# Performance work log

Measured on AMD Instinct MI355X. Metric: run time of the kernel, lower is better.

Reference implementation:

```python
import jax, jax.numpy as jnp
import numpy as np
import math

B, N, F = 4, 4096, 64
NEG_SLOPE = 0.01


def _leaky_relu(x):
    return jnp.where(x >= 0, x, NEG_SLOPE * x)


def setup_inputs() -> dict:
    key = jax.random.key(0)
    k1, k2, k3, k4, k5 = jax.random.split(key, 5)
    Q = jax.random.normal(k1, (B, N, F, 2), dtype=jnp.float32)
    K = jax.random.normal(k2, (B, N, F, 2), dtype=jnp.float32)
    V = jax.random.normal(k3, (B, N, F, 2), dtype=jnp.float32)
    W_att = jax.random.normal(k4, (F, F), dtype=jnp.float32) / math.sqrt(F)
    b_att = jax.random.normal(k5, (F,), dtype=jnp.float32) * 0.01
    return {"Q": Q, "K": K, "V": V, "W_att": W_att, "b_att": b_att}


def reference(Q, K, V, W_att, b_att):
    # Split complex components: last axis is (real, imag)
    Qr, Qi = Q[..., 0], Q[..., 1]
    Kr, Ki = K[..., 0], K[..., 1]
    Vr, Vi = V[..., 0], V[..., 1]

    n = Q.shape[1]
    scale = 1.0 / math.sqrt(n)  # num_nodes == N

    # Complex scores = Q @ K^T (no conjugation, as in torch einsum on complex)
    sr = (jnp.einsum('bik,bjk->bij', Qr, Kr) - jnp.einsum('bik,bjk->bij', Qi, Ki)) * scale
    si = (jnp.einsum('bik,bjk->bij', Qr, Ki) + jnp.einsum('bik,bjk->bij', Qi, Kr)) * scale

    # Causal mask: positions j > i are masked out (contribute zero weight)
    causal = jnp.tril(jnp.ones((n, n), dtype=bool))  # [N, N], True = keep
    wr = jnp.where(causal, _leaky_relu(sr), 0.0)
    wi = jnp.where(causal, _leaky_relu(si), 0.0)

    # Attention-weighted values (real weights with real V, imag with imag V)
    out_r = jnp.einsum('bij,bjf->bif', wr, Vr)
    out_i = jnp.einsum('bij,bjf->bif', wi, Vi)

    # att_map: shared linear layer
    out_r = out_r @ W_att.T + b_att
    out_i = out_i @ W_att.T + b_att

    return jnp.stack([out_r, out_i], axis=-1)  # [B, N, F, 2]
```

## Files before the change

### kernel.cpp

```cpp
#include <hip/hip_runtime.h>

#define NB 4
#define NN 4096
#define NF 64
#define TSTEP 8
#define BLKS_PER_B 260

typedef __attribute__((ext_vector_type(8))) short bf16x8;
typedef __attribute__((ext_vector_type(4))) float f32x4;

union S8 { unsigned short u[8]; bf16x8 v; };

__device__ __forceinline__ unsigned short f2bf(float x) {
    unsigned int uu = __builtin_bit_cast(unsigned int, x);
    uu += 0x7fffu + ((uu >> 16) & 1u);
    return (unsigned short)(uu >> 16);
}

__global__ __launch_bounds__(256)
void prep_all(const float* __restrict__ Q, const float* __restrict__ K,
              const float* __restrict__ V, const float* __restrict__ W,
              short* __restrict__ QF, short* __restrict__ KF,
              short* __restrict__ VF, short* __restrict__ WF,
              float* __restrict__ out) {
    int tid = blockIdx.x * 256 + threadIdx.x;

    if (tid < 262144) {
        int sel = tid >> 17;
        int r   = tid & 0x1FFFF;
        int l  = r & 63;
        int c  = (r >> 6) & 1;
        int rg = (r >> 7) & 255;
        int b  = r >> 15;
        const float* src = sel ? K : Q;
        short*       dst = sel ? KF : QF;

        int row = rg * 16 + (l & 15);
        int k0  = c * 32 + (l >> 4) * 8;
        const float4* s4 = (const float4*)src;
        int base4 = (b * NN + row) * 32 + (k0 >> 1);

        S8 ar, ai;
        #pragma unroll
        for (int m = 0; m < 4; ++m) {
            float4 f = s4[base4 + m];
            ar.u[2 * m]     = f2bf(f.x);
            ar.u[2 * m + 1] = f2bf(f.z);
            ai.u[2 * m]     = f2bf(f.y);
            ai.u[2 * m + 1] = f2bf(f.w);
        }
        int cid0 = ((b * 256 + rg) * 2 + c) * 2;
        *(bf16x8*)(dst + (cid0 + 0) * 512 + l * 8) = ar.v;
        *(bf16x8*)(dst + (cid0 + 1) * 512 + l * 8) = ai.v;
    } else if (tid < 393216) {
        int r = tid - 262144;
        int l  = r & 63;
        int c  = (r >> 6) & 1;
        int ft = (r >> 7) & 3;
        int jt = (r >> 9) & 63;
        int b  = (r >> 15) & 3;

        int f  = ft * 16 + (l & 15);
        int j0 = jt * 64 + c * 32 + (l >> 4) * 8;
        const float2* s2 = (const float2*)V;

        S8 ar, ai;
        #pragma unroll
        for (int e = 0; e < 8; ++e) {
            float2 g = s2[(b * NN + j0 + e) * 64 + f];
            ar.u[e] = f2bf(g.x);
            ai.u[e] = f2bf(g.y);
        }
        int cid0 = (((b * 64 + jt) * 4 + ft) * 2 + c) * 2;
        *(bf16x8*)(VF + (cid0 + 0) * 512 + l * 8) = ar.v;
        *(bf16x8*)(VF + (cid0 + 1) * 512 + l * 8) = ai.v;
    } else if (tid < 393728) {
        int r = tid - 393216;
        int l  = r & 63;
        int c  = (r >> 6) & 1;
        int ft = r >> 7;
        int row = ft * 16 + (l & 15);
        int k0  = c * 32 + (l >> 4) * 8;
        const float* sp = W + row * 64 + k0;
        S8 a;
        #pragma unroll
        for (int e = 0; e < 8; ++e) a.u[e] = f2bf(sp[e]);
        *(bf16x8*)(WF + ((ft * 2 + c) * 64 + l) * 8) = a.v;
    } else {
        int r = tid - 393728;
        float4 zz = {0.f, 0.f, 0.f, 0.f};
        ((float4*)out)[r] = zz;
    }
}

__device__ __forceinline__ int tri_inv(int g) {
    int it = (int)((__builtin_sqrtf(8.0f * (float)g + 1.0f) - 1.0f) * 0.5f);
    while ((it + 1) * (it + 2) / 2 <= g) ++it;
    while (it * (it + 1) / 2 > g) --it;
    return it;
}

__global__ __launch_bounds__(256, 4)
void attn_main(const short* __restrict__ QF, const short* __restrict__ KF,
               const short* __restrict__ VF, const short* __restrict__ WF,
               const float* __restrict__ batt, float* __restrict__ out) {
    __shared__ __align__(16) unsigned short wbuf[4][2048];

    int bid = blockIdx.x;
    int b   = bid / BLKS_PER_B;
    int g   = (bid % BLKS_PER_B) * TSTEP;
    int gend = g + TSTEP;

    int w   = threadIdx.x >> 6;
    int l   = threadIdx.x & 63;
    int r16 = l & 15;
    int lb  = l >> 4;

    const f32x4 z = {0.f, 0.f, 0.f, 0.f};
    const float SCALE = 1.0f / 64.0f;
    unsigned short* wb = wbuf[w];

    while (g < gend) {
        int it   = tri_inv(g);
        int base = it * (it + 1) / 2;
        int jt0  = g - base;
        int cnt  = min(gend - g, it + 1 - jt0);
        int jt1  = jt0 + cnt;

        bf16x8 qf[2][2];
        {
            int rg = it * 4 + w;
            #pragma unroll
            for (int c = 0; c < 2; ++c)
                #pragma unroll
                for (int ch = 0; ch < 2; ++ch)
                    qf[c][ch] = *(const bf16x8*)(QF + (((b * 256 + rg) * 2 + c) * 2 + ch) * 512 + l * 8);
        }

        f32x4 o[4][2];
        #pragma unroll
        for (int ft = 0; ft < 4; ++ft) { o[ft][0] = z; o[ft][1] = z; }

        for (int jt = jt0; jt < jt1; ++jt) {
            bool diag = (jt == it);
            #pragma unroll
            for (int ct = 0; ct < 4; ++ct) {
                bf16x8 kf[2][2];
                int rg = jt * 4 + ct;
                #pragma unroll
                for (int c = 0; c < 2; ++c)
                    #pragma unroll
                    for (int ch = 0; ch < 2; ++ch)
                        kf[c][ch] = *(const bf16x8*)(KF + (((b * 256 + rg) * 2 + c) * 2 + ch) * 512 + l * 8);

                f32x4 t1 = __builtin_amdgcn_mfma_f32_16x16x32_bf16(qf[0][0], kf[0][0], z, 0, 0, 0);
                t1 = __builtin_amdgcn_mfma_f32_16x16x32_bf16(qf[1][0], kf[1][0], t1, 0, 0, 0);
                f32x4 t2 = __builtin_amdgcn_mfma_f32_16x16x32_bf16(qf[0][1], kf[0][1], z, 0, 0, 0);
                t2 = __builtin_amdgcn_mfma_f32_16x16x32_bf16(qf[1][1], kf[1][1], t2, 0, 0, 0);
                f32x4 si = __builtin_amdgcn_mfma_f32_16x16x32_bf16(qf[0][0], kf[0][1], z, 0, 0, 0);
                si = __builtin_amdgcn_mfma_f32_16x16x32_bf16(qf[1][0], kf[1][1], si, 0, 0, 0);
                si = __builtin_amdgcn_mfma_f32_16x16x32_bf16(qf[0][1], kf[0][0], si, 0, 0, 0);
                si = __builtin_amdgcn_mfma_f32_16x16x32_bf16(qf[1][1], kf[1][0], si, 0, 0, 0);

                int cH  = ct >> 1;
                int lb2 = ((ct & 1) << 1) | (r16 >> 3);
                int e   = r16 & 7;
                int base_r = (cH * 2 + 0) * 512 + lb2 * 128 + lb * 32 + e;
                int base_i = (cH * 2 + 1) * 512 + lb2 * 128 + lb * 32 + e;
                #pragma unroll
                for (int reg = 0; reg < 4; ++reg) {
                    float sr = (t1[reg] - t2[reg]) * SCALE;
                    float sv = si[reg] * SCALE;
                    float wr = sr >= 0.f ? sr : 0.01f * sr;
                    float wi = sv >= 0.f ? sv : 0.01f * sv;
                    if (diag) {
                        int ig = w * 16 + lb * 4 + reg;
                        int jg = ct * 16 + r16;
                        if (jg > ig) { wr = 0.f; wi = 0.f; }
                    }
                    wb[base_r + reg * 8] = f2bf(wr);
                    wb[base_i + reg * 8] = f2bf(wi);
                }
            }

            bf16x8 wfr[2][2];
            #pragma unroll
            for (int c = 0; c < 2; ++c)
                #pragma unroll
                for (int ch = 0; ch < 2; ++ch)
                    wfr[c][ch] = *(const bf16x8*)(wb + (c * 2 + ch) * 512 + l * 8);

            #pragma unroll
            for (int ft = 0; ft < 4; ++ft) {
                #pragma unroll
                for (int ch = 0; ch < 2; ++ch) {
                    int cid0 = (((b * 64 + jt) * 4 + ft) * 2) * 2 + ch;
                    bf16x8 v0 = *(const bf16x8*)(VF + cid0 * 512 + l * 8);
                    bf16x8 v1 = *(const bf16x8*)(VF + (cid0 + 2) * 512 + l * 8);
                    o[ft][ch] = __builtin_amdgcn_mfma_f32_16x16x32_bf16(wfr[0][ch], v0, o[ft][ch], 0, 0, 0);
                    o[ft][ch] = __builtin_amdgcn_mfma_f32_16x16x32_bf16(wfr[1][ch], v1, o[ft][ch], 0, 0, 0);
                }
            }
        }

        #pragma unroll
        for (int ft = 0; ft < 4; ++ft) {
            int cH  = ft >> 1;
            int lb2 = ((ft & 1) << 1) | (r16 >> 3);
            int e   = r16 & 7;
            #pragma unroll
            for (int ch = 0; ch < 2; ++ch) {
                int bofs = (cH * 2 + ch) * 512 + lb2 * 128 + lb * 32 + e;
                #pragma unroll
                for (int reg = 0; reg < 4; ++reg)
                    wb[bofs + reg * 8] = f2bf(o[ft][ch][reg]);
            }
        }

        bf16x8 of[2][2];
        #pragma unroll
        for (int c = 0; c < 2; ++c)
            #pragma unroll
            for (int ch = 0; ch < 2; ++ch)
                of[c][ch] = *(const bf16x8*)(wb + (c * 2 + ch) * 512 + l * 8);

        bool whole = (jt0 == 0) && (jt1 == it + 1);
        bool addb  = (jt0 == 0);
        int ibase = b * NN + it * 64 + w * 16 + lb * 4;
        #pragma unroll
        for (int ft2 = 0; ft2 < 4; ++ft2) {
            bf16x8 wa0 = *(const bf16x8*)(WF + ((ft2 * 2 + 0) * 64 + l) * 8);
            bf16x8 wa1 = *(const bf16x8*)(WF + ((ft2 * 2 + 1) * 64 + l) * 8);
            float bb = addb ? batt[ft2 * 16 + r16] : 0.f;
            #pragma unroll
            for (int ch = 0; ch < 2; ++ch) {
                f32x4 acc = __builtin_amdgcn_mfma_f32_16x16x32_bf16(of[0][ch], wa0, z, 0, 0, 0);
                acc = __builtin_amdgcn_mfma_f32_16x16x32_bf16(of[1][ch], wa1, acc, 0, 0, 0);
                #pragma unroll
                for (int reg = 0; reg < 4; ++reg) {
                    int idx = ((ibase + reg) * 64 + ft2 * 16 + r16) * 2 + ch;
                    if (whole) out[idx] = acc[reg] + bb;
                    else       atomicAdd(out + idx, acc[reg] + bb);
                }
            }
        }

        g += cnt;
    }
}

extern "C" void kernel_launch(void* const* d_in, const int* in_sizes, int n_in,
                              void* d_out, int out_size, void* d_ws, size_t ws_size,
                              hipStream_t stream) {
    const float* Q  = (const float*)d_in[0];
    const float* K  = (const float*)d_in[1];
    const float* V  = (const float*)d_in[2];
    const float* W  = (const float*)d_in[3];
    const float* bA = (const float*)d_in[4];
    float* out = (float*)d_out;

    short* QF = (short*)d_ws;
    short* KF = QF + 2097152;
    short* VF = KF + 2097152;
    short* WF = VF + 2097152;

    prep_all<<<3586, 256, 0, stream>>>(Q, K, V, W, QF, KF, VF, WF, out);
    attn_main<<<NB * BLKS_PER_B, 256, 0, stream>>>(QF, KF, VF, WF, bA, out);
}
```

Baseline: 198.3 us.

## Keep attention weights in registers via transposed MFMA operands, drop LDS staging

Swaps the MFMA operand order so the score tile comes out transposed. The leaky-relu weights and the PV output can then be packed straight into bf16 B-operand registers, with no LDS round trip, and the V and W prep layouts are permuted to match. It folds the 1/64 scale into Q during prep, uses a branch-free leaky relu, and writes output with vectorised float4 stores. It also halves the per-block tile step, doubling the block count. The aim is to remove LDS writes and reads and improve store coalescing, at the cost of more atomics from the finer split.

```diff
diff --git a/kernel.cpp b/kernel.cpp
--- a/kernel.cpp
+++ b/kernel.cpp
@@ -3,8 +3,8 @@
 #define NB 4
 #define NN 4096
 #define NF 64
-#define TSTEP 8
-#define BLKS_PER_B 260
+#define TSTEP 4
+#define BLKS_PER_B 520
 
 typedef __attribute__((ext_vector_type(8))) short bf16x8;
 typedef __attribute__((ext_vector_type(4))) float f32x4;
@@ -34,6 +34,7 @@
         int b  = r >> 15;
         const float* src = sel ? K : Q;
         short*       dst = sel ? KF : QF;
+        float sc = sel ? 1.0f : 0.015625f;
 
         int row = rg * 16 + (l & 15);
         int k0  = c * 32 + (l >> 4) * 8;
@@ -44,10 +45,10 @@
         #pragma unroll
         for (int m = 0; m < 4; ++m) {
             float4 f = s4[base4 + m];
-            ar.u[2 * m]     = f2bf(f.x);
-            ar.u[2 * m + 1] = f2bf(f.z);
-            ai.u[2 * m]     = f2bf(f.y);
-            ai.u[2 * m + 1] = f2bf(f.w);
+            ar.u[2 * m]     = f2bf(f.x * sc);
+            ar.u[2 * m + 1] = f2bf(f.z * sc);
+            ai.u[2 * m]     = f2bf(f.y * sc);
+            ai.u[2 * m + 1] = f2bf(f.w * sc);
         }
         int cid0 = ((b * 256 + rg) * 2 + c) * 2;
         *(bf16x8*)(dst + (cid0 + 0) * 512 + l * 8) = ar.v;
@@ -61,15 +62,16 @@
         int b  = (r >> 15) & 3;
 
         int f  = ft * 16 + (l & 15);
-        int j0 = jt * 64 + c * 32 + (l >> 4) * 8;
+        int jb = jt * 64 + c * 32 + (l >> 4) * 4;
         const float2* s2 = (const float2*)V;
 
         S8 ar, ai;
         #pragma unroll
         for (int e = 0; e < 8; ++e) {
-            float2 g = s2[(b * NN + j0 + e) * 64 + f];
-            ar.u[e] = f2bf(g.x);
-            ai.u[e] = f2bf(g.y);
+            int j = jb + (e >> 2) * 16 + (e & 3);
+            float2 gg = s2[(b * NN + j) * 64 + f];
+            ar.u[e] = f2bf(gg.x);
+            ai.u[e] = f2bf(gg.y);
         }
         int cid0 = (((b * 64 + jt) * 4 + ft) * 2 + c) * 2;
         *(bf16x8*)(VF + (cid0 + 0) * 512 + l * 8) = ar.v;
@@ -78,14 +80,16 @@
         int r = tid - 393216;
         int l  = r & 63;
         int c  = (r >> 6) & 1;
-        int ft = r >> 7;
-        int row = ft * 16 + (l & 15);
-        int k0  = c * 32 + (l >> 4) * 8;
-        const float* sp = W + row * 64 + k0;
+        int gt = r >> 7;
+        int grow = gt * 16 + (l & 15);
+        const float* sp = W + grow * 64;
         S8 a;
         #pragma unroll
-        for (int e = 0; e < 8; ++e) a.u[e] = f2bf(sp[e]);
-        *(bf16x8*)(WF + ((ft * 2 + c) * 64 + l) * 8) = a.v;
+        for (int e = 0; e < 8; ++e) {
+            int f = c * 32 + (e >> 2) * 16 + (l >> 4) * 4 + (e & 3);
+            a.u[e] = f2bf(sp[f]);
+        }
+        *(bf16x8*)(WF + ((gt * 2 + c) * 64 + l) * 8) = a.v;
     } else {
         int r = tid - 393728;
         float4 zz = {0.f, 0.f, 0.f, 0.f};
@@ -104,8 +108,6 @@
 void attn_main(const short* __restrict__ QF, const short* __restrict__ KF,
                const short* __restrict__ VF, const short* __restrict__ WF,
                const float* __restrict__ batt, float* __restrict__ out) {
-    __shared__ __align__(16) unsigned short wbuf[4][2048];
-
     int bid = blockIdx.x;
     int b   = bid / BLKS_PER_B;
     int g   = (bid % BLKS_PER_B) * TSTEP;
@@ -117,8 +119,6 @@
     int lb  = l >> 4;
 
     const f32x4 z = {0.f, 0.f, 0.f, 0.f};
-    const float SCALE = 1.0f / 64.0f;
-    unsigned short* wb = wbuf[w];
 
     while (g < gend) {
         int it   = tri_inv(g);
@@ -129,12 +129,12 @@
 
         bf16x8 qf[2][2];
         {
-            int rg = it * 4 + w;
+            int rgq = it * 4 + w;
             #pragma unroll
             for (int c = 0; c < 2; ++c)
                 #pragma unroll
                 for (int ch = 0; ch < 2; ++ch)
-                    qf[c][ch] = *(const bf16x8*)(QF + (((b * 256 + rg) * 2 + c) * 2 + ch) * 512 + l * 8);
+                    qf[c][ch] = *(const bf16x8*)(QF + (((b * 256 + rgq) * 2 + c) * 2 + ch) * 512 + l * 8);
         }
 
         f32x4 o[4][2];
@@ -143,6 +143,8 @@
 
         for (int jt = jt0; jt < jt1; ++jt) {
             bool diag = (jt == it);
+            S8 pa[2][2];
+
             #pragma unroll
             for (int ct = 0; ct < 4; ++ct) {
                 bf16x8 kf[2][2];
@@ -153,94 +155,83 @@
                     for (int ch = 0; ch < 2; ++ch)
                         kf[c][ch] = *(const bf16x8*)(KF + (((b * 256 + rg) * 2 + c) * 2 + ch) * 512 + l * 8);
 
-                f32x4 t1 = __builtin_amdgcn_mfma_f32_16x16x32_bf16(qf[0][0], kf[0][0], z, 0, 0, 0);
-                t1 = __builtin_amdgcn_mfma_f32_16x16x32_bf16(qf[1][0], kf[1][0], t1, 0, 0, 0);
-                f32x4 t2 = __builtin_amdgcn_mfma_f32_16x16x32_bf16(qf[0][1], kf[0][1], z, 0, 0, 0);
-                t2 = __builtin_amdgcn_mfma_f32_16x16x32_bf16(qf[1][1], kf[1][1], t2, 0, 0, 0);
-                f32x4 si = __builtin_amdgcn_mfma_f32_16x16x32_bf16(qf[0][0], kf[0][1], z, 0, 0, 0);
-                si = __builtin_amdgcn_mfma_f32_16x16x32_bf16(qf[1][0], kf[1][1], si, 0, 0, 0);
-                si = __builtin_amdgcn_mfma_f32_16x16x32_bf16(qf[0][1], kf[0][0], si, 0, 0, 0);
-                si = __builtin_amdgcn_mfma_f32_16x16x32_bf16(qf[1][1], kf[1][0], si, 0, 0, 0);
-
-                int cH  = ct >> 1;
-                int lb2 = ((ct & 1) << 1) | (r16 >> 3);
-                int e   = r16 & 7;
-                int base_r = (cH * 2 + 0) * 512 + lb2 * 128 + lb * 32 + e;
-                int base_i = (cH * 2 + 1) * 512 + lb2 * 128 + lb * 32 + e;
+                f32x4 t1 = __builtin_amdgcn_mfma_f32_16x16x32_bf16(kf[0][0], qf[0][0], z, 0, 0, 0);
+                t1 = __builtin_amdgcn_mfma_f32_16x16x32_bf16(kf[1][0], qf[1][0], t1, 0, 0, 0);
+                f32x4 t2 = __builtin_amdgcn_mfma_f32_16x16x32_bf16(kf[0][1], qf[0][1], z, 0, 0, 0);
+                t2 = __builtin_amdgcn_mfma_f32_16x16x32_bf16(kf[1][1], qf[1][1], t2, 0, 0, 0);
+                f32x4 si = __builtin_amdgcn_mfma_f32_16x16x32_bf16(kf[0][1], qf[0][0], z, 0, 0, 0);
+                si = __builtin_amdgcn_mfma_f32_16x16x32_bf16(kf[1][1], qf[1][0], si, 0, 0, 0);
+                si = __builtin_amdgcn_mfma_f32_16x16x32_bf16(kf[0][0], qf[0][1], si, 0, 0, 0);
+                si = __builtin_amdgcn_mfma_f32_16x16x32_bf16(kf[1][0], qf[1][1], si, 0, 0, 0);
+
                 #pragma unroll
                 for (int reg = 0; reg < 4; ++reg) {
-                    float sr = (t1[reg] - t2[reg]) * SCALE;
-                    float sv = si[reg] * SCALE;
-                    float wr = sr >= 0.f ? sr : 0.01f * sr;
-                    float wi = sv >= 0.f ? sv : 0.01f * sv;
+                    float sr = t1[reg] - t2[reg];
+                    float sv = si[reg];
+                    float wr = fmaxf(sr, 0.f) + 0.01f * fminf(sr, 0.f);
+                    float wi = fmaxf(sv, 0.f) + 0.01f * fminf(sv, 0.f);
                     if (diag) {
-                        int ig = w * 16 + lb * 4 + reg;
-                        int jg = ct * 16 + r16;
+                        int jg = ct * 16 + lb * 4 + reg;
+                        int ig = w * 16 + r16;
                         if (jg > ig) { wr = 0.f; wi = 0.f; }
                     }
-                    wb[base_r + reg * 8] = f2bf(wr);
-                    wb[base_i + reg * 8] = f2bf(wi);
+                    pa[ct >> 1][0].u[(ct & 1) * 4 + reg] = f2bf(wr);
+                    pa[ct >> 1][1].u[(ct & 1) * 4 + reg] = f2bf(wi);
                 }
             }
 
-            bf16x8 wfr[2][2];
-            #pragma unroll
-            for (int c = 0; c < 2; ++c)
-                #pragma unroll
-                for (int ch = 0; ch < 2; ++ch)
-                    wfr[c][ch] = *(const bf16x8*)(wb + (c * 2 + ch) * 512 + l * 8);
-
             #pragma unroll
             for (int ft = 0; ft < 4; ++ft) {
                 #pragma unroll
                 for (int ch = 0; ch < 2; ++ch) {
-                    int cid0 = (((b * 64 + jt) * 4 + ft) * 2) * 2 + ch;
+                    int cid0 = (((b * 64 + jt) * 4 + ft) * 2 + 0) * 2 + ch;
                     bf16x8 v0 = *(const bf16x8*)(VF + cid0 * 512 + l * 8);
                     bf16x8 v1 = *(const bf16x8*)(VF + (cid0 + 2) * 512 + l * 8);
-                    o[ft][ch] = __builtin_amdgcn_mfma_f32_16x16x32_bf16(wfr[0][ch], v0, o[ft][ch], 0, 0, 0);
-                    o[ft][ch] = __builtin_amdgcn_mfma_f32_16x16x32_bf16(wfr[1][ch], v1, o[ft][ch], 0, 0, 0);
+                    o[ft][ch] = __builtin_amdgcn_mfma_f32_16x16x32_bf16(v0, pa[0][ch].v, o[ft][ch], 0, 0, 0);
+                    o[ft][ch] = __builtin_amdgcn_mfma_f32_16x16x32_bf16(v1, pa[1][ch].v, o[ft][ch], 0, 0, 0);
                 }
             }
         }
 
-        #pragma unroll
-        for (int ft = 0; ft < 4; ++ft) {
-            int cH  = ft >> 1;
-            int lb2 = ((ft & 1) << 1) | (r16 >> 3);
-            int e   = r16 & 7;
-            #pragma unroll
-            for (int ch = 0; ch < 2; ++ch) {
-                int bofs = (cH * 2 + ch) * 512 + lb2 * 128 + lb * 32 + e;
-                #pragma unroll
-                for (int reg = 0; reg < 4; ++reg)
-                    wb[bofs + reg * 8] = f2bf(o[ft][ch][reg]);
-            }
-        }
-
-        bf16x8 of[2][2];
-        #pragma unroll
-        for (int c = 0; c < 2; ++c)
+        S8 ob[2][2];
+        #pragma unroll
+        for (int cc = 0; cc < 2; ++cc)
             #pragma unroll
             for (int ch = 0; ch < 2; ++ch)
-                of[c][ch] = *(const bf16x8*)(wb + (c * 2 + ch) * 512 + l * 8);
+                #pragma unroll
+                for (int s = 0; s < 2; ++s)
+                    #pragma unroll
+                    for (int reg = 0; reg < 4; ++reg)
+                        ob[cc][ch].u[s * 4 + reg] = f2bf(o[cc * 2 + s][ch][reg]);
 
         bool whole = (jt0 == 0) && (jt1 == it + 1);
         bool addb  = (jt0 == 0);
-        int ibase = b * NN + it * 64 + w * 16 + lb * 4;
-        #pragma unroll
-        for (int ft2 = 0; ft2 < 4; ++ft2) {
-            bf16x8 wa0 = *(const bf16x8*)(WF + ((ft2 * 2 + 0) * 64 + l) * 8);
-            bf16x8 wa1 = *(const bf16x8*)(WF + ((ft2 * 2 + 1) * 64 + l) * 8);
-            float bb = addb ? batt[ft2 * 16 + r16] : 0.f;
-            #pragma unroll
-            for (int ch = 0; ch < 2; ++ch) {
-                f32x4 acc = __builtin_amdgcn_mfma_f32_16x16x32_bf16(of[0][ch], wa0, z, 0, 0, 0);
-                acc = __builtin_amdgcn_mfma_f32_16x16x32_bf16(of[1][ch], wa1, acc, 0, 0, 0);
+        int obase0 = ((b * NN + it * 64 + w * 16 + r16) * 64) * 2;
+
+        #pragma unroll
+        for (int gt = 0; gt < 4; ++gt) {
+            bf16x8 wa0 = *(const bf16x8*)(WF + ((gt * 2 + 0) * 64 + l) * 8);
+            bf16x8 wa1 = *(const bf16x8*)(WF + ((gt * 2 + 1) * 64 + l) * 8);
+            float4 bq = *(const float4*)(batt + gt * 16 + lb * 4);
+            float bbv[4] = {bq.x, bq.y, bq.z, bq.w};
+
+            f32x4 a0 = __builtin_amdgcn_mfma_f32_16x16x32_bf16(wa0, ob[0][0].v, z, 0, 0, 0);
+            a0 = __builtin_amdgcn_mfma_f32_16x16x32_bf16(wa1, ob[1][0].v, a0, 0, 0, 0);
+            f32x4 a1 = __builtin_amdgcn_mfma_f32_16x16x32_bf16(wa0, ob[0][1].v, z, 0, 0, 0);
+            a1 = __builtin_amdgcn_mfma_f32_16x16x32_bf16(wa1, ob[1][1].v, a1, 0, 0, 0);
+
+            int obase = obase0 + (gt * 16 + lb * 4) * 2;
+            if (whole) {
+                float4 sA = {a0[0] + bbv[0], a1[0] + bbv[0], a0[1] + bbv[1], a1[1] + bbv[1]};
+                float4 sB = {a0[2] + bbv[2], a1[2] + bbv[2], a0[3] + bbv[3], a1[3] + bbv[3]};
+                *(float4*)(out + obase)     = sA;
+                *(float4*)(out + obase + 4) = sB;
+            } else {
                 #pragma unroll
                 for (int reg = 0; reg < 4; ++reg) {
-                    int idx = ((ibase + reg) * 64 + ft2 * 16 + r16) * 2 + ch;
-                    if (whole) out[idx] = acc[reg] + bb;
-                    else       atomicAdd(out + idx, acc[reg] + bb);
+                    float bb = addb ? bbv[reg] : 0.f;
+                    atomicAdd(out + obase + reg * 2,     a0[reg] + bb);
+                    atomicAdd(out + obase + reg * 2 + 1, a1[reg] + bb);
                 }
             }
         }
```

Result: slower. 573.3 us (+189.2%).
